# Kernel optimization log

Hardware: AMD Instinct MI355X
Metric: run time of the kernel (lower is better)

## Reference

```python
import jax, jax.numpy as jnp
import numpy as np

B = 256      # graph pairs
N = 256      # nodes per graph (uniform -> padding is a reshape)
DEG = 16     # avg degree
D = 32       # one_hot_dim
F1, F2, F3 = 128, 64, 64
T = 16       # tensor_neurons
BINS = 16
BOT = 16     # bottle_neck_neurons


def setup_inputs() -> dict:
    key = jax.random.key(0)
    ks = jax.random.split(key, 24)
    NT = B * N            # total nodes per side
    NE = B * N * DEG      # total directed edges per side
    x_q = jax.random.normal(ks[0], (NT, D), jnp.float32)
    x_c = jax.random.normal(ks[1], (NT, D), jnp.float32)
    edge_q = jax.random.randint(ks[2], (2, NE), 0, NT, jnp.int32)
    edge_c = jax.random.randint(ks[3], (2, NE), 0, NT, jnp.int32)
    qgraph_sizes = jnp.full((B,), N, jnp.int32)
    cgraph_sizes = jnp.full((B,), N, jnp.int32)

    def glorot(k, shape):
        fan = sum(shape[-2:]) if len(shape) >= 2 else shape[0] * 2
        return jax.random.uniform(k, shape, jnp.float32, -1.0, 1.0) * np.sqrt(6.0 / fan)

    params = dict(
        W1=glorot(ks[4], (D, F1)), b1=jnp.zeros((F1,), jnp.float32),
        W2=glorot(ks[5], (F1, F2)), b2=jnp.zeros((F2,), jnp.float32),
        W3=glorot(ks[6], (F2, F3)), b3=jnp.zeros((F3,), jnp.float32),
        attn_w=glorot(ks[7], (F3, F3)),
        ntn_a_w=glorot(ks[8], (T, F3, F3)),
        ntn_b_w=glorot(ks[9], (2 * F3, T)),
        ntn_bias=glorot(ks[10], (T, 1)),
        fc1_w=glorot(ks[11], (T + BINS, BOT)), fc1_b=jnp.zeros((BOT,), jnp.float32),
        fc2_w=glorot(ks[12], (BOT, 1)), fc2_b=jnp.zeros((1,), jnp.float32),
    )
    return dict(x_q=x_q, edge_q=edge_q, x_c=x_c, edge_c=edge_c,
                qgraph_sizes=qgraph_sizes, cgraph_sizes=cgraph_sizes, **params)


def _gcn(x, src, dst, W, b):
    n = x.shape[0]
    h = x @ W
    loop = jnp.arange(n, dtype=src.dtype)
    s = jnp.concatenate([src, loop])
    d = jnp.concatenate([dst, loop])
    deg = jax.ops.segment_sum(jnp.ones(s.shape, h.dtype), d, num_segments=n)
    dinv = jnp.where(deg > 0, jax.lax.rsqrt(jnp.maximum(deg, 1.0)), 0.0)
    coef = (dinv[s] * dinv[d])[:, None]
    return jax.ops.segment_sum(h[s] * coef, d, num_segments=n) + b


def _gnn(x, ei, W1, b1, W2, b2, W3, b3):
    src, dst = ei[0], ei[1]
    h = jax.nn.relu(_gcn(x, src, dst, W1, b1))        # dropout is identity in eval
    h = jax.nn.relu(_gcn(h, src, dst, W2, b2))
    return _gcn(h, src, dst, W3, b3)                  # [B*N, F3]


def _att_pool(q, attn_w, sizes):
    # q: [B, N, F3]
    ctx = jnp.tanh((q.sum(axis=1) @ attn_w) / sizes.astype(q.dtype)[:, None])  # [B, F3]
    sig = jax.nn.sigmoid(jnp.einsum('bnf,bf->bn', q, ctx))                      # [B, N]
    return jnp.einsum('bnf,bn->bf', q, sig)                                     # [B, F3]


def _pair_hist(q, c):
    # per-pair histogram of q @ c^T with BINS bins over each pair's [min, max]
    s = jax.lax.stop_gradient(jnp.einsum('bnf,bmf->bnm', q, c))  # [B, N, N]
    mn = s.min(axis=(1, 2), keepdims=True)
    mx = s.max(axis=(1, 2), keepdims=True)
    idx = jnp.clip(jnp.floor((s - mn) / jnp.maximum(mx - mn, 1e-12) * BINS),
                   0, BINS - 1).astype(jnp.int32)
    gid = (idx + jnp.arange(B, dtype=jnp.int32)[:, None, None] * BINS).reshape(-1)
    h = jax.ops.segment_sum(jnp.ones(gid.shape, jnp.float32), gid,
                            num_segments=B * BINS).reshape(B, BINS)
    return h / h.sum(axis=1, keepdims=True)


def reference(x_q, edge_q, x_c, edge_c, qgraph_sizes, cgraph_sizes,
              W1, b1, W2, b2, W3, b3, attn_w, ntn_a_w, ntn_b_w, ntn_bias,
              fc1_w, fc1_b, fc2_w, fc2_b):
    q = _gnn(x_q, edge_q, W1, b1, W2, b2, W3, b3).reshape(B, N, F3)
    c = _gnn(x_c, edge_c, W1, b1, W2, b2, W3, b3).reshape(B, N, F3)
    e1 = _att_pool(q, attn_w, qgraph_sizes)
    e2 = _att_pool(c, attn_w, cgraph_sizes)
    ntn = (jnp.einsum('bi,tij,bj->bt', e1, ntn_a_w, e2)
           + jnp.concatenate([e1, e2], axis=-1) @ ntn_b_w
           + ntn_bias[:, 0])
    scores = jax.nn.relu(ntn)                                   # [B, T]
    hist = _pair_hist(q, c)                                     # [B, BINS]
    scores = jnp.concatenate([scores, hist], axis=1)
    scores = jax.nn.relu(scores @ fc1_w + fc1_b)
    p = jax.nn.sigmoid(scores @ fc2_w + fc2_b)[:, 0]            # [B]
    ged = -0.5 * (qgraph_sizes + cgraph_sizes).astype(p.dtype) * jnp.log(p)
    return ged
```

## Files before the change

kernel.cpp:

```cpp
#include <hip/hip_runtime.h>
#include <hip/hip_bf16.h>
#include <math.h>

#define BB 256
#define NN 256
#define NT (BB*NN)
#define NT2 (2*NT)
#define NE (NT*16)
#define DD 32
#define F1C 128
#define F2C 64
#define F3C 64
#define TT 16
#define BINS 16

#define NBUCK 256
#define BSHIFT 9
#define BNODES 512
#define BCAP 10240
#define EPB 4096

typedef __attribute__((ext_vector_type(8))) short short8;
typedef __attribute__((ext_vector_type(4))) float f32x4;
typedef __attribute__((ext_vector_type(2))) float f32x2;

__device__ inline float b2f(ushort u) { return __uint_as_float(((uint)u) << 16); }
__device__ inline ushort f2b(float f) {
    uint u = __float_as_uint(f);
    return (ushort)((u + 0x7fffu + ((u >> 16) & 1u)) >> 16);
}
__device__ inline float clamp8(float v) { return fminf(fmaxf(v, -448.0f), 448.0f); }
__device__ inline uchar f2f8(float v) {
    int r = __builtin_amdgcn_cvt_pk_fp8_f32(clamp8(v), 0.0f, 0, false);
    return (uchar)(r & 0xff);
}
__device__ inline void f8x8_acc(uint2 w, float* acc) {
    f32x2 p;
    p = __builtin_amdgcn_cvt_pk_f32_fp8(w.x, false); acc[0] += p.x; acc[1] += p.y;
    p = __builtin_amdgcn_cvt_pk_f32_fp8(w.x, true);  acc[2] += p.x; acc[3] += p.y;
    p = __builtin_amdgcn_cvt_pk_f32_fp8(w.y, false); acc[4] += p.x; acc[5] += p.y;
    p = __builtin_amdgcn_cvt_pk_f32_fp8(w.y, true);  acc[6] += p.x; acc[7] += p.y;
}
__device__ inline uint2 f8x8_pack(const float* v) {
    uint2 r;
    r.x = (uint)__builtin_amdgcn_cvt_pk_fp8_f32(clamp8(v[0]), clamp8(v[1]), 0, false);
    r.x = (uint)__builtin_amdgcn_cvt_pk_fp8_f32(clamp8(v[2]), clamp8(v[3]), (int)r.x, true);
    r.y = (uint)__builtin_amdgcn_cvt_pk_fp8_f32(clamp8(v[4]), clamp8(v[5]), 0, false);
    r.y = (uint)__builtin_amdgcn_cvt_pk_fp8_f32(clamp8(v[6]), clamp8(v[7]), (int)r.y, true);
    return r;
}

__global__ __launch_bounds__(256) void zero_k(int* __restrict__ gcount) {
    gcount[threadIdx.x] = 0;
}

__global__ __launch_bounds__(256) void p1cvt_k(const int* __restrict__ eq, const int* __restrict__ ec,
                                               uint* __restrict__ staged, int* __restrict__ gcount,
                                               const float* __restrict__ W1, const float* __restrict__ W2,
                                               const float* __restrict__ W3, ushort* __restrict__ Wt1,
                                               ushort* __restrict__ Wt2, uchar* __restrict__ Wt3f8) {
    int t = threadIdx.x;
    if (blockIdx.x < 512) {
        __shared__ uint s_pk[EPB];
        __shared__ int s_cnt[NBUCK];
        __shared__ int s_off[NBUCK];
        __shared__ int s_base[NBUCK];
        __shared__ int s_gb[NBUCK];
        bool sideB = blockIdx.x >= 256;
        const int* edge = sideB ? ec : eq;
        int off = sideB ? NT : 0;
        int e0 = (blockIdx.x & 255) * EPB;
        s_cnt[t] = 0;
        __syncthreads();
        uint pk[16]; int bk[16];
#pragma unroll
        for (int j = 0; j < 16; j++) {
            int e = e0 + j * 256 + t;
            int s = edge[e] + off;
            int d = edge[NE + e] + off;
            bk[j] = d >> BSHIFT;
            pk[j] = ((uint)s << BSHIFT) | (uint)(d & (BNODES - 1));
            atomicAdd(&s_cnt[bk[j]], 1);
        }
        __syncthreads();
        s_off[t] = s_cnt[t];
        __syncthreads();
        for (int o = 1; o < NBUCK; o <<= 1) {
            int x = (t >= o) ? s_off[t - o] : 0;
            __syncthreads();
            s_off[t] += x;
            __syncthreads();
        }
        {
            int ex = s_off[t] - s_cnt[t];
            s_base[t] = ex;
            s_off[t] = ex;
            s_gb[t] = atomicAdd(&gcount[t], s_cnt[t]);
        }
        __syncthreads();
#pragma unroll
        for (int j = 0; j < 16; j++) {
            int pos = atomicAdd(&s_off[bk[j]], 1);
            s_pk[pos] = pk[j];
        }
        __syncthreads();
        int w = t >> 6, l = t & 63;
        int bsel = l >> 4, l16 = l & 15;
        for (int pb = w; pb < NBUCK / 4; pb += 4) {
            int bkt = pb * 4 + bsel;
            int n = s_cnt[bkt], st = s_base[bkt], gb = s_gb[bkt];
            if (gb + n > BCAP) n = max(0, BCAP - gb);
            for (int i = l16; i < n; i += 16)
                staged[bkt * BCAP + gb + i] = s_pk[st + i];
        }
    } else {
        int i = (blockIdx.x - 512) * 256 + t;
        if (i < DD * F1C)  { int k = i / F1C, n = i % F1C; Wt1[n * DD + k]  = f2b(W1[i]); }
        if (i < F1C * F2C) { int k = i / F2C, n = i % F2C; Wt2[n * F1C + k] = f2b(W2[i]); }
        if (i < F2C * F3C) { int k = i / F3C, n = i % F3C; Wt3f8[n * F2C + k] = f2f8(W3[i]); }
    }
}

__global__ __launch_bounds__(256) void csr_p2_k(const uint* __restrict__ staged, const int* __restrict__ gcount,
                                                int* __restrict__ rp, int* __restrict__ indeg,
                                                float* __restrict__ dinv, int* __restrict__ ep,
                                                const float* __restrict__ xq, const float* __restrict__ xc,
                                                ushort* __restrict__ xb) {
    int b = blockIdx.x;
    int t = threadIdx.x;
    __shared__ int cnt[BNODES];
    __shared__ int fl[BNODES];
    __shared__ int wsum[256];
    __shared__ int gsc[NBUCK];
    __shared__ float sdv[BNODES];
    cnt[t] = 0; cnt[t + 256] = 0;
    gsc[t] = min(gcount[t], BCAP);
    __syncthreads();
    for (int off = 1; off < NBUCK; off <<= 1) {
        int x = (t >= off) ? gsc[t - off] : 0;
        __syncthreads();
        gsc[t] += x;
        __syncthreads();
    }
    int gbase = (b == 0) ? 0 : gsc[b - 1];
    int n = min(gcount[b], BCAP);
    const uint* sb = staged + (size_t)b * BCAP;
    int i = t;
    for (; i + 768 < n; i += 1024) {
        uint p0 = sb[i];
        uint p1 = sb[i + 256];
        uint p2 = sb[i + 512];
        uint p3 = sb[i + 768];
        atomicAdd(&cnt[p0 & (BNODES - 1)], 1);
        atomicAdd(&cnt[p1 & (BNODES - 1)], 1);
        atomicAdd(&cnt[p2 & (BNODES - 1)], 1);
        atomicAdd(&cnt[p3 & (BNODES - 1)], 1);
    }
    for (; i < n; i += 256)
        atomicAdd(&cnt[sb[i] & (BNODES - 1)], 1);
    __syncthreads();
    int base2 = t * 2;
    int c0 = cnt[base2], c1 = cnt[base2 + 1];
    int s2 = c0 + c1;
    wsum[t] = s2;
    __syncthreads();
    for (int off = 1; off < 256; off <<= 1) {
        int x = (t >= off) ? wsum[t - off] : 0;
        __syncthreads();
        wsum[t] += x;
        __syncthreads();
    }
    int p = gbase + wsum[t] - s2;
    int v0 = b * BNODES + base2;
    float d0 = rsqrtf((float)(c0 + 1));
    float d1 = rsqrtf((float)(c1 + 1));
    rp[v0] = p;          fl[base2] = p;
    indeg[v0] = c0;      dinv[v0] = d0;      sdv[base2] = d0;
    p += c0;
    rp[v0 + 1] = p;      fl[base2 + 1] = p;
    indeg[v0 + 1] = c1;  dinv[v0 + 1] = d1;  sdv[base2 + 1] = d1;
    __syncthreads();
    i = t;
    for (; i + 768 < n; i += 1024) {
        uint p0 = sb[i];
        uint p1 = sb[i + 256];
        uint p2 = sb[i + 512];
        uint p3 = sb[i + 768];
        ep[atomicAdd(&fl[p0 & (BNODES - 1)], 1)] = (int)(p0 >> BSHIFT);
        ep[atomicAdd(&fl[p1 & (BNODES - 1)], 1)] = (int)(p1 >> BSHIFT);
        ep[atomicAdd(&fl[p2 & (BNODES - 1)], 1)] = (int)(p2 >> BSHIFT);
        ep[atomicAdd(&fl[p3 & (BNODES - 1)], 1)] = (int)(p3 >> BSHIFT);
    }
    for (; i < n; i += 256) {
        uint pk = sb[i];
        ep[atomicAdd(&fl[pk & (BNODES - 1)], 1)] = (int)(pk >> BSHIFT);
    }
    {
        const float* xs = (b < 128) ? (xq + (size_t)b * BNODES * DD)
                                    : (xc + ((size_t)b * BNODES - NT) * DD);
        ushort* xd = xb + (size_t)b * BNODES * DD;
        for (int g = t; g < BNODES * DD / 4; g += 256) {
            int r = g >> 3;
            float4 v = ((const float4*)xs)[g];
            float dv = sdv[r];
            ushort4 o;
            o.x = f2b(v.x * dv); o.y = f2b(v.y * dv);
            o.z = f2b(v.z * dv); o.w = f2b(v.w * dv);
            ((ushort4*)xd)[g] = o;
        }
    }
}

__global__ __launch_bounds__(256) void agg_bf_k(const ushort* __restrict__ in, const int* __restrict__ rp,
                                                const int* __restrict__ indeg, const int* __restrict__ ep,
                                                const float* __restrict__ dinv,
                                                ushort* __restrict__ out) {
    int g = threadIdx.x >> 2;
    int l = threadIdx.x & 3;
    int v = blockIdx.x * 64 + g;
    float dv = dinv[v];
    short8 rs = *(const short8*)(in + (size_t)v * 32 + l * 8);
    float acc[8];
#pragma unroll
    for (int j = 0; j < 8; j++) acc[j] = b2f((ushort)rs[j]);
    int start = rp[v];
    int cnt   = indeg[v];
    int i = 0;
    for (; i + 4 <= cnt; i += 4) {
        int s0 = ep[start + i];
        int s1 = ep[start + i + 1];
        int s2 = ep[start + i + 2];
        int s3 = ep[start + i + 3];
        short8 r0 = *(const short8*)(in + (size_t)s0 * 32 + l * 8);
        short8 r1 = *(const short8*)(in + (size_t)s1 * 32 + l * 8);
        short8 r2 = *(const short8*)(in + (size_t)s2 * 32 + l * 8);
        short8 r3 = *(const short8*)(in + (size_t)s3 * 32 + l * 8);
#pragma unroll
        for (int j = 0; j < 8; j++) {
            acc[j] += b2f((ushort)r0[j]);
            acc[j] += b2f((ushort)r1[j]);
            acc[j] += b2f((ushort)r2[j]);
            acc[j] += b2f((ushort)r3[j]);
        }
    }
    for (; i < cnt; i++) {
        int s0 = ep[start + i];
        short8 r0 = *(const short8*)(in + (size_t)s0 * 32 + l * 8);
#pragma unroll
        for (int j = 0; j < 8; j++) acc[j] += b2f((ushort)r0[j]);
    }
    short8 o;
#pragma unroll
    for (int j = 0; j < 8; j++) o[j] = (short)f2b(dv * acc[j]);
    *(short8*)(out + (size_t)v * 32 + l * 8) = o;
}

template<bool OUT_BF16, bool BIAS, bool RELU>
__global__ __launch_bounds__(256) void agg_f8_k(const uchar* __restrict__ in, const int* __restrict__ rp,
                                                const int* __restrict__ indeg, const int* __restrict__ ep,
                                                const float* __restrict__ dinv,
                                                const float* __restrict__ bias, void* __restrict__ outp) {
    int g = threadIdx.x >> 3;
    int l = threadIdx.x & 7;
    int v = blockIdx.x * 32 + g;
    float dv = dinv[v];
    float acc[8] = {0, 0, 0, 0, 0, 0, 0, 0};
    f8x8_acc(*(const uint2*)(in + (size_t)v * 64 + l * 8), acc);
    int start = rp[v];
    int cnt   = indeg[v];
    int i = 0;
    for (; i + 8 <= cnt; i += 8) {
        int sx[8];
#pragma unroll
        for (int j = 0; j < 8; j++) sx[j] = ep[start + i + j];
        uint2 gx[8];
#pragma unroll
        for (int j = 0; j < 8; j++) gx[j] = *(const uint2*)(in + (size_t)sx[j] * 64 + l * 8);
#pragma unroll
        for (int j = 0; j < 8; j++) f8x8_acc(gx[j], acc);
    }
    for (; i + 4 <= cnt; i += 4) {
        int s0 = ep[start + i];
        int s1 = ep[start + i + 1];
        int s2 = ep[start + i + 2];
        int s3 = ep[start + i + 3];
        uint2 g0 = *(const uint2*)(in + (size_t)s0 * 64 + l * 8);
        uint2 g1 = *(const uint2*)(in + (size_t)s1 * 64 + l * 8);
        uint2 g2 = *(const uint2*)(in + (size_t)s2 * 64 + l * 8);
        uint2 g3 = *(const uint2*)(in + (size_t)s3 * 64 + l * 8);
        f8x8_acc(g0, acc); f8x8_acc(g1, acc); f8x8_acc(g2, acc); f8x8_acc(g3, acc);
    }
    for (; i < cnt; i++) {
        int s0 = ep[start + i];
        f8x8_acc(*(const uint2*)(in + (size_t)s0 * 64 + l * 8), acc);
    }
#pragma unroll
    for (int j = 0; j < 8; j++) {
        float x = dv * acc[j];
        if (BIAS) x += bias[l * 8 + j];
        if (RELU) x = fmaxf(x, 0.0f);
        acc[j] = x;
    }
    if (OUT_BF16) {
        short8 o;
#pragma unroll
        for (int j = 0; j < 8; j++) o[j] = (short)f2b(acc[j]);
        *(short8*)((ushort*)outp + (size_t)v * 64 + l * 8) = o;
    } else {
        *(uint2*)((uchar*)outp + (size_t)v * 64 + l * 8) = f8x8_pack(acc);
    }
}

__global__ __launch_bounds__(256) void gemm12_k(const ushort* __restrict__ xa,
                                                const ushort* __restrict__ Wt1,
                                                const float* __restrict__ b1,
                                                const ushort* __restrict__ Wt2,
                                                const float* __restrict__ dinv,
                                                uchar* __restrict__ h8a) {
    __shared__ ushort s_h1[128][136];
    int w = threadIdx.x >> 6, lane = threadIdx.x & 63;
    int r16 = lane & 15, quad = lane >> 4, koff = quad * 8;
    size_t rows0 = (size_t)blockIdx.x * 128;

    short8 af1[2];
#pragma unroll
    for (int mt = 0; mt < 2; mt++)
        af1[mt] = *(const short8*)(xa + (rows0 + (w * 2 + mt) * 16 + r16) * 32 + koff);
#pragma unroll
    for (int nt = 0; nt < 8; nt++) {
        short8 bfr = *(const short8*)(Wt1 + (size_t)(nt * 16 + r16) * 32 + koff);
        f32x4 acc[2] = {{0.f,0.f,0.f,0.f},{0.f,0.f,0.f,0.f}};
        acc[0] = __builtin_amdgcn_mfma_f32_16x16x32_bf16(af1[0], bfr, acc[0], 0, 0, 0);
        acc[1] = __builtin_amdgcn_mfma_f32_16x16x32_bf16(af1[1], bfr, acc[1], 0, 0, 0);
        int col = nt * 16 + r16;
        float bc = b1[col];
#pragma unroll
        for (int mt = 0; mt < 2; mt++)
#pragma unroll
            for (int r = 0; r < 4; r++) {
                int rl = (w * 2 + mt) * 16 + quad * 4 + r;
                s_h1[rl][col] = f2b(fmaxf(acc[mt][r] + bc, 0.0f));
            }
    }
    __syncthreads();

    short8 af2[4][2];
#pragma unroll
    for (int kc = 0; kc < 4; kc++)
#pragma unroll
        for (int mt = 0; mt < 2; mt++)
            af2[kc][mt] = *(const short8*)&s_h1[(w * 2 + mt) * 16 + r16][kc * 32 + koff];
    float dvr[2][4];
#pragma unroll
    for (int mt = 0; mt < 2; mt++)
#pragma unroll
        for (int r = 0; r < 4; r++)
            dvr[mt][r] = dinv[rows0 + (w * 2 + mt) * 16 + quad * 4 + r];
#pragma unroll
    for (int nt = 0; nt < 4; nt++) {
        f32x4 acc[2] = {{0.f,0.f,0.f,0.f},{0.f,0.f,0.f,0.f}};
#pragma unroll
        for (int kc = 0; kc < 4; kc++) {
            short8 bfr = *(const short8*)(Wt2 + (size_t)(nt * 16 + r16) * 128 + kc * 32 + koff);
            acc[0] = __builtin_amdgcn_mfma_f32_16x16x32_bf16(af2[kc][0], bfr, acc[0], 0, 0, 0);
            acc[1] = __builtin_amdgcn_mfma_f32_16x16x32_bf16(af2[kc][1], bfr, acc[1], 0, 0, 0);
        }
#pragma unroll
        for (int mt = 0; mt < 2; mt++)
#pragma unroll
            for (int r = 0; r < 4; r++) {
                size_t row = rows0 + (w * 2 + mt) * 16 + quad * 4 + r;
                int col = nt * 16 + r16;
                h8a[row * 64 + col] = f2f8(acc[mt][r] * dvr[mt][r]);
            }
    }
}

__global__ __launch_bounds__(256) void gemm_f8_k(const uchar* __restrict__ A8,
                                                 const uchar* __restrict__ Wt8,
                                                 const float* __restrict__ dinv,
                                                 uchar* __restrict__ out8) {
    int w = threadIdx.x >> 6, lane = threadIdx.x & 63;
    int r16 = lane & 15, koff = (lane >> 4) * 8;
    size_t rows0 = (size_t)blockIdx.x * 128;

    long af[2][2];
#pragma unroll
    for (int kc = 0; kc < 2; kc++)
#pragma unroll
        for (int mt = 0; mt < 2; mt++)
            af[kc][mt] = *(const long*)(A8 + (rows0 + (w * 2 + mt) * 16 + r16) * 64 + kc * 32 + koff);

    float dvr[2][4];
#pragma unroll
    for (int mt = 0; mt < 2; mt++)
#pragma unroll
        for (int r = 0; r < 4; r++)
            dvr[mt][r] = dinv[rows0 + (w * 2 + mt) * 16 + (lane >> 4) * 4 + r];

#pragma unroll
    for (int nt = 0; nt < 4; nt++) {
        f32x4 acc[2] = {{0.f,0.f,0.f,0.f},{0.f,0.f,0.f,0.f}};
#pragma unroll
        for (int kc = 0; kc < 2; kc++) {
            long b = *(const long*)(Wt8 + (size_t)(nt * 16 + r16) * 64 + kc * 32 + koff);
            acc[0] = __builtin_amdgcn_mfma_f32_16x16x32_fp8_fp8(af[kc][0], b, acc[0], 0, 0, 0);
            acc[1] = __builtin_amdgcn_mfma_f32_16x16x32_fp8_fp8(af[kc][1], b, acc[1], 0, 0, 0);
        }
#pragma unroll
        for (int mt = 0; mt < 2; mt++) {
#pragma unroll
            for (int r = 0; r < 4; r++) {
                size_t row = rows0 + (w * 2 + mt) * 16 + (lane >> 4) * 4 + r;
                int col = nt * 16 + (lane & 15);
                out8[row * 64 + col] = f2f8(acc[mt][r] * dvr[mt][r]);
            }
        }
    }
}

__global__ __launch_bounds__(1024) void tail_k(const ushort* __restrict__ fin,
                                               const int* __restrict__ qsz, const int* __restrict__ csz,
                                               const float* __restrict__ attn_w,
                                               const float* __restrict__ A, const float* __restrict__ bw,
                                               const float* __restrict__ ntn_bias,
                                               const float* __restrict__ fc1w, const float* __restrict__ fc1b,
                                               const float* __restrict__ fc2w, const float* __restrict__ fc2b,
                                               float* __restrict__ out) {
    __shared__ ushort q_s[256][72];
    __shared__ ushort c_s[256][72];
    __shared__ ushort h[16 * 1024];
    __shared__ int hp[16 * 64];
    __shared__ float s_red[16 * 64];
    __shared__ float s_sq[64], s_ctx[64], s_sig[256];
    __shared__ float smn[16], smx[16], s_sc[2];
    __shared__ float s_e1[64], s_e2[64];
    __shared__ float s_ntn[16], s_s[32], s_a[16];
    __shared__ int s_hist[16];

    int b = blockIdx.x;
    int t = threadIdx.x;
    int f = t & 63;
    int w = t >> 6;
    int r16 = f & 15, koff = (f >> 4) * 8;
    const ushort* qb = fin + (size_t)b * NN * 64;
    const ushort* cb = fin + (size_t)(NT + b * NN) * 64;

#pragma unroll
    for (int it = 0; it < 2; it++) {
        int idx = it * 8192 + t * 8;
        int row = idx >> 6, f0 = idx & 63;
        *(short8*)&q_s[row][f0] = *(const short8*)(qb + idx);
        *(short8*)&c_s[row][f0] = *(const short8*)(cb + idx);
    }
    __syncthreads();

    short8 a[2];
    {
        int qrow = w * 16 + r16;
        a[0] = *(const short8*)&q_s[qrow][koff];
        a[1] = *(const short8*)&q_s[qrow][32 + koff];
    }
    float mn = 1e30f, mx = -1e30f;
    for (int mt = 0; mt < 16; mt++) {
        int crow = mt * 16 + r16;
        short8 b0 = *(const short8*)&c_s[crow][koff];
        short8 b1 = *(const short8*)&c_s[crow][32 + koff];
        f32x4 acc = {0.0f, 0.0f, 0.0f, 0.0f};
        acc = __builtin_amdgcn_mfma_f32_16x16x32_bf16(a[0], b0, acc, 0, 0, 0);
        acc = __builtin_amdgcn_mfma_f32_16x16x32_bf16(a[1], b1, acc, 0, 0, 0);
        mn = fminf(mn, fminf(fminf(acc[0], acc[1]), fminf(acc[2], acc[3])));
        mx = fmaxf(mx, fmaxf(fmaxf(acc[0], acc[1]), fmaxf(acc[2], acc[3])));
    }
    for (int off = 32; off; off >>= 1) {
        mn = fminf(mn, __shfl_xor(mn, off, 64));
        mx = fmaxf(mx, __shfl_xor(mx, off, 64));
    }
    if (f == 0) { smn[w] = mn; smx[w] = mx; }
    __syncthreads();
    if (t == 0) {
        float m0 = smn[0], m1 = smx[0];
#pragma unroll
        for (int j = 1; j < 16; j++) {
            m0 = fminf(m0, smn[j]);
            m1 = fmaxf(m1, smx[j]);
        }
        s_sc[0] = m0;
        s_sc[1] = 16.0f / fmaxf(m1 - m0, 1e-12f);
    }
#pragma unroll
    for (int i = 0; i < 16; i++) h[i * 1024 + t] = 0;
    __syncthreads();
    float bmn = s_sc[0], bscale = s_sc[1];
    for (int mt = 0; mt < 16; mt++) {
        int crow = mt * 16 + r16;
        short8 b0 = *(const short8*)&c_s[crow][koff];
        short8 b1 = *(const short8*)&c_s[crow][32 + koff];
        f32x4 acc = {0.0f, 0.0f, 0.0f, 0.0f};
        acc = __builtin_amdgcn_mfma_f32_16x16x32_bf16(a[0], b0, acc, 0, 0, 0);
        acc = __builtin_amdgcn_mfma_f32_16x16x32_bf16(a[1], b1, acc, 0, 0, 0);
#pragma unroll
        for (int r = 0; r < 4; r++) {
            int bin = (int)floorf((acc[r] - bmn) * bscale);
            bin = min(max(bin, 0), 15);
            h[bin * 1024 + t] += 1;
        }
    }
    __syncthreads();
    {
        int bb = t >> 6, part = t & 63;
        int sum = 0;
#pragma unroll
        for (int j = 0; j < 16; j++) sum += (int)h[bb * 1024 + part * 16 + j];
        hp[bb * 64 + part] = sum;
    }
    __syncthreads();
    if (t < 16) {
        int s = 0;
#pragma unroll
        for (int j = 0; j < 64; j++) s += hp[t * 64 + j];
        s_hist[t] = s;
    }

    {
        float psum = 0.0f;
#pragma unroll 8
        for (int i2 = 0; i2 < 16; i2++) psum += b2f(q_s[w * 16 + i2][f]);
        s_red[w * 64 + f] = psum;
        __syncthreads();
        if (w == 0) {
            float s = 0.0f;
#pragma unroll
            for (int j = 0; j < 16; j++) s += s_red[j * 64 + f];
            s_sq[f] = s;
            float acc = 0.0f;
            for (int k = 0; k < 64; k++) acc += s_sq[k] * attn_w[k * 64 + f];
            s_ctx[f] = tanhf(acc / (float)qsz[b]);
        }
        __syncthreads();
        if (t < 256) {
            float acc = 0.0f;
#pragma unroll 8
            for (int k = 0; k < 64; k++) acc += b2f(q_s[t][k]) * s_ctx[k];
            s_sig[t] = 1.0f / (1.0f + expf(-acc));
        }
        __syncthreads();
        float eacc = 0.0f;
#pragma unroll 8
        for (int i = 0; i < 16; i++) {
            int n = w * 16 + i;
            eacc += s_sig[n] * b2f(q_s[n][f]);
        }
        s_red[w * 64 + f] = eacc;
        __syncthreads();
        if (w == 0) {
            float s = 0.0f;
#pragma unroll
            for (int j = 0; j < 16; j++) s += s_red[j * 64 + f];
            s_e1[f] = s;
        }
    }
    __syncthreads();

    {
        float psum = 0.0f;
#pragma unroll 8
        for (int i2 = 0; i2 < 16; i2++) psum += b2f(c_s[w * 16 + i2][f]);
        s_red[w * 64 + f] = psum;
        __syncthreads();
        if (w == 0) {
            float s = 0.0f;
#pragma unroll
            for (int j = 0; j < 16; j++) s += s_red[j * 64 + f];
            s_sq[f] = s;
            float acc = 0.0f;
            for (int k = 0; k < 64; k++) acc += s_sq[k] * attn_w[k * 64 + f];
            s_ctx[f] = tanhf(acc / (float)csz[b]);
        }
        __syncthreads();
        if (t < 256) {
            float acc = 0.0f;
#pragma unroll 8
            for (int k = 0; k < 64; k++) acc += b2f(c_s[t][k]) * s_ctx[k];
            s_sig[t] = 1.0f / (1.0f + expf(-acc));
        }
        __syncthreads();
        float eacc = 0.0f;
#pragma unroll 8
        for (int i = 0; i < 16; i++) {
            int n = w * 16 + i;
            eacc += s_sig[n] * b2f(c_s[n][f]);
        }
        s_red[w * 64 + f] = eacc;
        __syncthreads();
        if (w == 0) {
            float s = 0.0f;
#pragma unroll
            for (int j = 0; j < 16; j++) s += s_red[j * 64 + f];
            s_e2[f] = s;
        }
    }
    __syncthreads();

    {
        const float4* Ar = (const float4*)(A + (size_t)t * 64);
        float acc = 0.0f;
#pragma unroll
        for (int j = 0; j < 16; j++) {
            float4 a4 = Ar[j];
            acc += a4.x * s_e2[4 * j] + a4.y * s_e2[4 * j + 1]
                 + a4.z * s_e2[4 * j + 2] + a4.w * s_e2[4 * j + 3];
        }
        float p = s_e1[f] * acc;
        for (int off = 32; off; off >>= 1) p += __shfl_xor(p, off, 64);
        if (f == 0) s_ntn[w] = p;
    }
    __syncthreads();
    if (t < 16) {
        float acc = s_ntn[t] + ntn_bias[t];
        for (int k = 0; k < 64; k++) acc += s_e1[k] * bw[k * 16 + t];
        for (int k = 0; k < 64; k++) acc += s_e2[k] * bw[(64 + k) * 16 + t];
        s_s[t] = fmaxf(acc, 0.0f);
        s_s[16 + t] = (float)s_hist[t] * (1.0f / 65536.0f);
    }
    __syncthreads();
    if (t < 16) {
        float aa = fc1b[t];
        for (int k = 0; k < 32; k++) aa += s_s[k] * fc1w[k * 16 + t];
        s_a[t] = fmaxf(aa, 0.0f);
    }
    __syncthreads();
    if (t == 0) {
        float z = fc2b[0];
        for (int j = 0; j < 16; j++) z += s_a[j] * fc2w[j];
        float nz = -z;
        float sp = (nz > 20.0f) ? nz : log1pf(expf(nz));
        out[b] = 0.5f * (float)(qsz[b] + csz[b]) * sp;
    }
}

extern "C" void kernel_launch(void* const* d_in, const int* in_sizes, int n_in,
                              void* d_out, int out_size, void* d_ws, size_t ws_size,
                              hipStream_t stream) {
    const float* x_q    = (const float*)d_in[0];
    const int*   edge_q = (const int*)d_in[1];
    const float* x_c    = (const float*)d_in[2];
    const int*   edge_c = (const int*)d_in[3];
    const int*   qsz    = (const int*)d_in[4];
    const int*   csz    = (const int*)d_in[5];
    const float* W1 = (const float*)d_in[6];
    const float* b1 = (const float*)d_in[7];
    const float* W2 = (const float*)d_in[8];
    const float* b2 = (const float*)d_in[9];
    const float* W3 = (const float*)d_in[10];
    const float* b3 = (const float*)d_in[11];
    const float* attn_w  = (const float*)d_in[12];
    const float* ntn_a   = (const float*)d_in[13];
    const float* ntn_b   = (const float*)d_in[14];
    const float* ntn_bias= (const float*)d_in[15];
    const float* fc1w = (const float*)d_in[16];
    const float* fc1b = (const float*)d_in[17];
    const float* fc2w = (const float*)d_in[18];
    const float* fc2b = (const float*)d_in[19];
    float* out = (float*)d_out;

    char* w = (char*)d_ws;
    auto alloc = [&](size_t bytes) -> void* {
        void* p = (void*)w;
        w += (bytes + 255) & ~(size_t)255;
        return p;
    };
    int*    rp     = (int*)alloc((size_t)NT2 * 4);
    int*    indeg  = (int*)alloc((size_t)NT2 * 4);
    float*  dinv   = (float*)alloc((size_t)NT2 * 4);
    int*    gcount = (int*)alloc(NBUCK * 4);
    uint*   staged = (uint*)alloc((size_t)NBUCK * BCAP * 4);
    int*    ep     = (int*)alloc((size_t)2 * NE * 4);
    ushort* xb     = (ushort*)alloc((size_t)NT2 * 32 * 2);
    ushort* xa     = (ushort*)alloc((size_t)NT2 * 32 * 2);
    uchar*  h8a    = (uchar*)alloc((size_t)NT2 * 64);
    uchar*  h8b    = (uchar*)alloc((size_t)NT2 * 64);
    ushort* fin    = (ushort*)alloc((size_t)NT2 * 64 * 2);
    ushort* Wt1    = (ushort*)alloc((size_t)DD * F1C * 2);
    ushort* Wt2    = (ushort*)alloc((size_t)F1C * F2C * 2);
    uchar*  Wt3f8  = (uchar*)alloc((size_t)F2C * F3C);

    zero_k<<<1, 256, 0, stream>>>(gcount);
    p1cvt_k<<<512 + 32, 256, 0, stream>>>(edge_q, edge_c, staged, gcount,
                                          W1, W2, W3, Wt1, Wt2, Wt3f8);
    csr_p2_k<<<NBUCK, 256, 0, stream>>>(staged, gcount, rp, indeg, dinv, ep,
                                        x_q, x_c, xb);

    agg_bf_k<<<NT2 / 64, 256, 0, stream>>>(xb, rp, indeg, ep, dinv, xa);
    gemm12_k<<<NT2 / 128, 256, 0, stream>>>(xa, Wt1, b1, Wt2, dinv, h8a);
    agg_f8_k<false, true, true><<<NT2 / 32, 256, 0, stream>>>(h8a, rp, indeg, ep, dinv, b2, h8b);
    gemm_f8_k<<<NT2 / 128, 256, 0, stream>>>(h8b, Wt3f8, dinv, h8a);
    agg_f8_k<true, true, false><<<NT2 / 32, 256, 0, stream>>>(h8a, rp, indeg, ep, dinv, b3, fin);

    tail_k<<<BB, 1024, 0, stream>>>(fin, qsz, csz, attn_w, ntn_a, ntn_b, ntn_bias,
                                    fc1w, fc1b, fc2w, fc2b, out);
}
```

Measured before the change: 275.8 us.

## Run q and c attention pooling concurrently and interleave with histogram phases

The tail kernel now splits its 16 waves into two halves, one for the query side and one for the corpus side, so both attention-pooling reductions run at the same time. These stages are interleaved with the min/max and histogram MFMA passes, so they share barriers instead of running as separate serial phases. This removes roughly ten block-wide barriers and keeps otherwise idle waves busy. In exchange each wave does more per-thread reduction work (32 rows instead of 16) and needs extra shared memory for the per-side buffers.

```diff
diff --git a/kernel.cpp b/kernel.cpp
--- a/kernel.cpp
+++ b/kernel.cpp
@@ -431,10 +431,10 @@
     __shared__ ushort c_s[256][72];
     __shared__ ushort h[16 * 1024];
     __shared__ int hp[16 * 64];
-    __shared__ float s_red[16 * 64];
-    __shared__ float s_sq[64], s_ctx[64], s_sig[256];
+    __shared__ float s_red[2][512];
+    __shared__ float s_sq2[2][64], s_ctx2[2][64], s_sig2[2][256];
     __shared__ float smn[16], smx[16], s_sc[2];
-    __shared__ float s_e1[64], s_e2[64];
+    __shared__ float s_e[2][64];
     __shared__ float s_ntn[16], s_s[32], s_a[16];
     __shared__ int s_hist[16];
 
@@ -443,6 +443,9 @@
     int f = t & 63;
     int w = t >> 6;
     int r16 = f & 15, koff = (f >> 4) * 8;
+    int side = w >> 3;
+    int w8 = w & 7;
+    ushort (*tile)[72] = side ? c_s : q_s;
     const ushort* qb = fin + (size_t)b * NN * 64;
     const ushort* cb = fin + (size_t)(NT + b * NN) * 64;
 
@@ -455,29 +458,38 @@
     }
     __syncthreads();
 
-    short8 a[2];
+    short8 a0, a1;
     {
         int qrow = w * 16 + r16;
-        a[0] = *(const short8*)&q_s[qrow][koff];
-        a[1] = *(const short8*)&q_s[qrow][32 + koff];
-    }
-    float mn = 1e30f, mx = -1e30f;
-    for (int mt = 0; mt < 16; mt++) {
-        int crow = mt * 16 + r16;
-        short8 b0 = *(const short8*)&c_s[crow][koff];
-        short8 b1 = *(const short8*)&c_s[crow][32 + koff];
-        f32x4 acc = {0.0f, 0.0f, 0.0f, 0.0f};
-        acc = __builtin_amdgcn_mfma_f32_16x16x32_bf16(a[0], b0, acc, 0, 0, 0);
-        acc = __builtin_amdgcn_mfma_f32_16x16x32_bf16(a[1], b1, acc, 0, 0, 0);
-        mn = fminf(mn, fminf(fminf(acc[0], acc[1]), fminf(acc[2], acc[3])));
-        mx = fmaxf(mx, fmaxf(fmaxf(acc[0], acc[1]), fmaxf(acc[2], acc[3])));
-    }
-    for (int off = 32; off; off >>= 1) {
-        mn = fminf(mn, __shfl_xor(mn, off, 64));
-        mx = fmaxf(mx, __shfl_xor(mx, off, 64));
-    }
-    if (f == 0) { smn[w] = mn; smx[w] = mx; }
-    __syncthreads();
+        a0 = *(const short8*)&q_s[qrow][koff];
+        a1 = *(const short8*)&q_s[qrow][32 + koff];
+    }
+    {
+        float mn = 1e30f, mx = -1e30f;
+        for (int mt = 0; mt < 16; mt++) {
+            int crow = mt * 16 + r16;
+            short8 b0 = *(const short8*)&c_s[crow][koff];
+            short8 b1 = *(const short8*)&c_s[crow][32 + koff];
+            f32x4 acc = {0.0f, 0.0f, 0.0f, 0.0f};
+            acc = __builtin_amdgcn_mfma_f32_16x16x32_bf16(a0, b0, acc, 0, 0, 0);
+            acc = __builtin_amdgcn_mfma_f32_16x16x32_bf16(a1, b1, acc, 0, 0, 0);
+            mn = fminf(mn, fminf(fminf(acc[0], acc[1]), fminf(acc[2], acc[3])));
+            mx = fmaxf(mx, fmaxf(fmaxf(acc[0], acc[1]), fmaxf(acc[2], acc[3])));
+        }
+        for (int off = 32; off; off >>= 1) {
+            mn = fminf(mn, __shfl_xor(mn, off, 64));
+            mx = fmaxf(mx, __shfl_xor(mx, off, 64));
+        }
+        if (f == 0) { smn[w] = mn; smx[w] = mx; }
+    }
+    {
+        float psum = 0.0f;
+#pragma unroll 8
+        for (int i2 = 0; i2 < 32; i2++) psum += b2f(tile[w8 * 32 + i2][f]);
+        s_red[side][w8 * 64 + f] = psum;
+    }
+    __syncthreads();
+
     if (t == 0) {
         float m0 = smn[0], m1 = smx[0];
 #pragma unroll
@@ -488,25 +500,48 @@
         s_sc[0] = m0;
         s_sc[1] = 16.0f / fmaxf(m1 - m0, 1e-12f);
     }
+    if (w8 == 0) {
+        float s = 0.0f;
+#pragma unroll
+        for (int j = 0; j < 8; j++) s += s_red[side][j * 64 + f];
+        s_sq2[side][f] = s;
+        float acc = 0.0f;
+        for (int k = 0; k < 64; k++) acc += s_sq2[side][k] * attn_w[k * 64 + f];
+        float sz = (float)((side ? csz : qsz)[b]);
+        s_ctx2[side][f] = tanhf(acc / sz);
+    }
 #pragma unroll
     for (int i = 0; i < 16; i++) h[i * 1024 + t] = 0;
     __syncthreads();
-    float bmn = s_sc[0], bscale = s_sc[1];
-    for (int mt = 0; mt < 16; mt++) {
-        int crow = mt * 16 + r16;
-        short8 b0 = *(const short8*)&c_s[crow][koff];
-        short8 b1 = *(const short8*)&c_s[crow][32 + koff];
-        f32x4 acc = {0.0f, 0.0f, 0.0f, 0.0f};
-        acc = __builtin_amdgcn_mfma_f32_16x16x32_bf16(a[0], b0, acc, 0, 0, 0);
-        acc = __builtin_amdgcn_mfma_f32_16x16x32_bf16(a[1], b1, acc, 0, 0, 0);
-#pragma unroll
-        for (int r = 0; r < 4; r++) {
-            int bin = (int)floorf((acc[r] - bmn) * bscale);
-            bin = min(max(bin, 0), 15);
-            h[bin * 1024 + t] += 1;
-        }
-    }
-    __syncthreads();
+
+    {
+        float bmn = s_sc[0], bscale = s_sc[1];
+        for (int mt = 0; mt < 16; mt++) {
+            int crow = mt * 16 + r16;
+            short8 b0 = *(const short8*)&c_s[crow][koff];
+            short8 b1 = *(const short8*)&c_s[crow][32 + koff];
+            f32x4 acc = {0.0f, 0.0f, 0.0f, 0.0f};
+            acc = __builtin_amdgcn_mfma_f32_16x16x32_bf16(a0, b0, acc, 0, 0, 0);
+            acc = __builtin_amdgcn_mfma_f32_16x16x32_bf16(a1, b1, acc, 0, 0, 0);
+#pragma unroll
+            for (int r = 0; r < 4; r++) {
+                int bin = (int)floorf((acc[r] - bmn) * bscale);
+                bin = min(max(bin, 0), 15);
+                h[bin * 1024 + t] += 1;
+            }
+        }
+    }
+    {
+        int lt = t & 511;
+        if (lt < 256) {
+            float acc = 0.0f;
+#pragma unroll 8
+            for (int k = 0; k < 64; k++) acc += b2f(tile[lt][k]) * s_ctx2[side][k];
+            s_sig2[side][lt] = 1.0f / (1.0f + expf(-acc));
+        }
+    }
+    __syncthreads();
+
     {
         int bb = t >> 6, part = t & 63;
         int sum = 0;
@@ -514,91 +549,28 @@
         for (int j = 0; j < 16; j++) sum += (int)h[bb * 1024 + part * 16 + j];
         hp[bb * 64 + part] = sum;
     }
-    __syncthreads();
+    {
+        float eacc = 0.0f;
+#pragma unroll 8
+        for (int i = 0; i < 32; i++) {
+            int n = w8 * 32 + i;
+            eacc += s_sig2[side][n] * b2f(tile[n][f]);
+        }
+        s_red[side][w8 * 64 + f] = eacc;
+    }
+    __syncthreads();
+
     if (t < 16) {
         int s = 0;
 #pragma unroll
         for (int j = 0; j < 64; j++) s += hp[t * 64 + j];
         s_hist[t] = s;
     }
-
-    {
-        float psum = 0.0f;
-#pragma unroll 8
-        for (int i2 = 0; i2 < 16; i2++) psum += b2f(q_s[w * 16 + i2][f]);
-        s_red[w * 64 + f] = psum;
-        __syncthreads();
-        if (w == 0) {
-            float s = 0.0f;
-#pragma unroll
-            for (int j = 0; j < 16; j++) s += s_red[j * 64 + f];
-            s_sq[f] = s;
-            float acc = 0.0f;
-            for (int k = 0; k < 64; k++) acc += s_sq[k] * attn_w[k * 64 + f];
-            s_ctx[f] = tanhf(acc / (float)qsz[b]);
-        }
-        __syncthreads();
-        if (t < 256) {
-            float acc = 0.0f;
-#pragma unroll 8
-            for (int k = 0; k < 64; k++) acc += b2f(q_s[t][k]) * s_ctx[k];
-            s_sig[t] = 1.0f / (1.0f + expf(-acc));
-        }
-        __syncthreads();
-        float eacc = 0.0f;
-#pragma unroll 8
-        for (int i = 0; i < 16; i++) {
-            int n = w * 16 + i;
-            eacc += s_sig[n] * b2f(q_s[n][f]);
-        }
-        s_red[w * 64 + f] = eacc;
-        __syncthreads();
-        if (w == 0) {
-            float s = 0.0f;
-#pragma unroll
-            for (int j = 0; j < 16; j++) s += s_red[j * 64 + f];
-            s_e1[f] = s;
-        }
-    }
-    __syncthreads();
-
-    {
-        float psum = 0.0f;
-#pragma unroll 8
-        for (int i2 = 0; i2 < 16; i2++) psum += b2f(c_s[w * 16 + i2][f]);
-        s_red[w * 64 + f] = psum;
-        __syncthreads();
-        if (w == 0) {
-            float s = 0.0f;
-#pragma unroll
-            for (int j = 0; j < 16; j++) s += s_red[j * 64 + f];
-            s_sq[f] = s;
-            float acc = 0.0f;
-            for (int k = 0; k < 64; k++) acc += s_sq[k] * attn_w[k * 64 + f];
-            s_ctx[f] = tanhf(acc / (float)csz[b]);
-        }
-        __syncthreads();
-        if (t < 256) {
-            float acc = 0.0f;
-#pragma unroll 8
-            for (int k = 0; k < 64; k++) acc += b2f(c_s[t][k]) * s_ctx[k];
-            s_sig[t] = 1.0f / (1.0f + expf(-acc));
-        }
-        __syncthreads();
-        float eacc = 0.0f;
-#pragma unroll 8
-        for (int i = 0; i < 16; i++) {
-            int n = w * 16 + i;
-            eacc += s_sig[n] * b2f(c_s[n][f]);
-        }
-        s_red[w * 64 + f] = eacc;
-        __syncthreads();
-        if (w == 0) {
-            float s = 0.0f;
-#pragma unroll
-            for (int j = 0; j < 16; j++) s += s_red[j * 64 + f];
-            s_e2[f] = s;
-        }
+    if (w8 == 0) {
+        float s = 0.0f;
+#pragma unroll
+        for (int j = 0; j < 8; j++) s += s_red[side][j * 64 + f];
+        s_e[side][f] = s;
     }
     __syncthreads();
 
@@ -608,18 +580,18 @@
 #pragma unroll
         for (int j = 0; j < 16; j++) {
             float4 a4 = Ar[j];
-            acc += a4.x * s_e2[4 * j] + a4.y * s_e2[4 * j + 1]
-                 + a4.z * s_e2[4 * j + 2] + a4.w * s_e2[4 * j + 3];
-        }
-        float p = s_e1[f] * acc;
+            acc += a4.x * s_e[1][4 * j] + a4.y * s_e[1][4 * j + 1]
+                 + a4.z * s_e[1][4 * j + 2] + a4.w * s_e[1][4 * j + 3];
+        }
+        float p = s_e[0][f] * acc;
         for (int off = 32; off; off >>= 1) p += __shfl_xor(p, off, 64);
         if (f == 0) s_ntn[w] = p;
     }
     __syncthreads();
     if (t < 16) {
         float acc = s_ntn[t] + ntn_bias[t];
-        for (int k = 0; k < 64; k++) acc += s_e1[k] * bw[k * 16 + t];
-        for (int k = 0; k < 64; k++) acc += s_e2[k] * bw[(64 + k) * 16 + t];
+        for (int k = 0; k < 64; k++) acc += s_e[0][k] * bw[k * 16 + t];
+        for (int k = 0; k < 64; k++) acc += s_e[1][k] * bw[(64 + k) * 16 + t];
         s_s[t] = fmaxf(acc, 0.0f);
         s_s[16 + t] = (float)s_hist[t] * (1.0f / 65536.0f);
     }
```

Measured after the change: 277.5 us. About the same (+0.6%).
